# Kernel optimization log

Hardware: AMD Instinct MI355X
Metric: run time of the kernel (lower is better)

## Reference

```python
import jax, jax.numpy as jnp
import numpy as np

DIM = 64  # QK head dim, matches init kwarg 'dim'

def setup_inputs() -> dict:
    key = jax.random.key(0)
    kq, kk, kv = jax.random.split(key, 3)
    B, L, C, D, H = 2, 2048, 16, DIM, 64
    query = jax.random.normal(kq, (B, L, C, D), dtype=jnp.float32)
    k_ = jax.random.normal(kk, (B, L, C, D), dtype=jnp.float32)
    value = jax.random.normal(kv, (B, L, C, H), dtype=jnp.float32)
    return {"query": query, "key": k_, "value": value}

def reference(query, key, value):
    scaler = 1.0 / jnp.sqrt(jnp.float32(DIM))
    # score: [b, c, l, m]
    score = jnp.einsum('blcd,bmcd->bclm', query, key) * scaler
    # mask=False, dropout=0 -> identity
    attn = jax.nn.softmax(score, axis=3)
    # out: [b, l, c, h]
    out = jnp.einsum('bmch,bclm->blch', value, attn)
    return out
```

## Files before the change

kernel.cpp:

```cpp
#include <hip/hip_runtime.h>
#include <hip/hip_bf16.h>
#include <stdint.h>

#define B_ 2
#define L_ 2048
#define C_ 16
#define D_ 64
#define H_ 64
#define QBLK 128
#define KVBLK 64
#define NTILES 32
#define NTHREADS 256
#define NHEADS 32
#define TILE_ELEMS 4096
#define TENSOR_ELEMS (NHEADS * NTILES * TILE_ELEMS)

typedef __attribute__((ext_vector_type(8))) short bf16x8;
typedef __attribute__((ext_vector_type(16))) float f32x16;
typedef __attribute__((ext_vector_type(8))) unsigned short u16x8;

__device__ inline unsigned short f2bf(float f) {
  union { float f; unsigned int u; } v; v.f = f;
  unsigned int u = v.u;
  unsigned int r = (u + 0x7FFFu + ((u >> 16) & 1u)) >> 16;
  return (unsigned short)r;
}

__device__ inline float fast_exp2(float x) {
#if __has_builtin(__builtin_amdgcn_exp2f)
  return __builtin_amdgcn_exp2f(x);
#else
  return exp2f(x);
#endif
}

__device__ inline unsigned cvt_pk_bf16(float lo, float hi) {
  unsigned r;
  asm("v_cvt_pk_bf16_f32 %0, %1, %2" : "=v"(r) : "v"(lo), "v"(hi));
  return r;
}

__device__ inline void pl32swap(unsigned &x, unsigned &y) {
#if __has_builtin(__builtin_amdgcn_permlane32_swap)
  auto r = __builtin_amdgcn_permlane32_swap(x, y, false, false);
  x = r[0]; y = r[1];
#else
  asm("v_permlane32_swap_b32 %0, %1" : "+v"(x), "+&v"(y));
#endif
}

__device__ inline float xsum32(float v) {
  unsigned x = __float_as_uint(v), y = x;
  pl32swap(x, y);
  return __uint_as_float(x) + __uint_as_float(y);
}

__global__ __launch_bounds__(256) void prepack_kernel(
    const float* __restrict__ Kg, const float* __restrict__ Vg,
    unsigned short* __restrict__ Kb, unsigned short* __restrict__ Vb) {
  int idx = blockIdx.x * 256 + threadIdx.x;
  if (idx < 524288) {
    int i = idx;
    int lane = i & 63, frag = (i >> 6) & 7, t = (i >> 9) & 31, head = i >> 14;
    int b = head >> 4, c = head & 15;
    int ks = frag >> 1, half = frag & 1;
    int row = half * 32 + (lane & 31);
    int kb = ks * 16 + (lane >> 5) * 8;
    const float* src = Kg + ((size_t)(b * L_ + t * 64 + row) * C_ + c) * D_ + kb;
    float4 a0 = ((const float4*)src)[0];
    float4 a1 = ((const float4*)src)[1];
    u16x8 pk;
    pk[0] = f2bf(a0.x); pk[1] = f2bf(a0.y); pk[2] = f2bf(a0.z); pk[3] = f2bf(a0.w);
    pk[4] = f2bf(a1.x); pk[5] = f2bf(a1.y); pk[6] = f2bf(a1.z); pk[7] = f2bf(a1.w);
    size_t dst = ((((size_t)(head * 32 + t)) * 8 + frag) * 64 + lane) * 8;
    *(u16x8*)&Kb[dst] = pk;
  } else {
    int i = idx - 524288;
    int lane = i & 63, frag = (i >> 6) & 7, t = (i >> 9) & 31, head = i >> 14;
    int b = head >> 4, c = head & 15;
    int m = frag >> 1, half = frag & 1;
    int h = half * 32 + (lane & 31);
    int kv0 = m * 16 + (lane >> 5) * 8;
    const float* src = Vg + ((size_t)(b * L_ + t * 64 + kv0) * C_ + c) * H_ + h;
    u16x8 pv;
#pragma unroll
    for (int j = 0; j < 8; ++j) pv[j] = f2bf(src[(size_t)j * C_ * H_]);
    size_t dst = ((((size_t)(head * 32 + t)) * 8 + frag) * 64 + lane) * 8;
    *(u16x8*)&Vb[dst] = pv;
  }
}

__global__ __launch_bounds__(NTHREADS, 2) void attn_fwd_kernel(
    const float* __restrict__ Qg,
    const unsigned short* __restrict__ Kb,
    const unsigned short* __restrict__ Vb,
    float* __restrict__ Og) {
  const int tid  = threadIdx.x;
  const int lane = tid & 63;
  const int w    = tid >> 6;
  const int ql   = lane & 31;
  const int u    = lane >> 5;

  const int bid   = blockIdx.x;
  const int swz   = (bid & 7) * 64 + (bid >> 3);
  const int head  = swz >> 4;
  const int qtile = swz & 15;
  const int b     = head >> 4;
  const int c     = head & 15;
  const int q0    = qtile * QBLK;

  const unsigned short* KbL = Kb + (size_t)head * NTILES * TILE_ELEMS + lane * 8;
  const unsigned short* VbL = Vb + (size_t)head * NTILES * TILE_ELEMS + lane * 8;

  const float sc2 = 0.125f * 1.44269504088896340736f;
  const int qr = q0 + w * 32 + ql;
  const float* qrow = Qg + ((size_t)(b * L_ + qr) * C_ + c) * D_;
  bf16x8 qf[4];
#pragma unroll
  for (int ks = 0; ks < 4; ++ks) {
    float4 a0 = *(const float4*)(qrow + ks * 16 + u * 8);
    float4 a1 = *(const float4*)(qrow + ks * 16 + u * 8 + 4);
    bf16x8 q8;
    q8[0] = (short)f2bf(a0.x * sc2); q8[1] = (short)f2bf(a0.y * sc2);
    q8[2] = (short)f2bf(a0.z * sc2); q8[3] = (short)f2bf(a0.w * sc2);
    q8[4] = (short)f2bf(a1.x * sc2); q8[5] = (short)f2bf(a1.y * sc2);
    q8[6] = (short)f2bf(a1.z * sc2); q8[7] = (short)f2bf(a1.w * sc2);
    qf[ks] = q8;
  }

  f32x16 o0, o1;
#pragma unroll
  for (int i = 0; i < 16; ++i) { o0[i] = 0.f; o1[i] = 0.f; }
  float l_own = 0.f;

  bf16x8 kfr[8], vfr[8];
#pragma unroll
  for (int f = 0; f < 8; ++f) kfr[f] = *(const bf16x8*)(KbL + (size_t)f * 512);
#pragma unroll
  for (int f = 0; f < 8; ++f) vfr[f] = *(const bf16x8*)(VbL + (size_t)f * 512);

  for (int t = 0; t < NTILES; ++t) {
    const int tl = (t + 1 < NTILES) ? (t + 1) : t;

    f32x16 s0, s1;
#pragma unroll
    for (int i = 0; i < 16; ++i) { s0[i] = 0.f; s1[i] = 0.f; }
    __builtin_amdgcn_s_setprio(1);
#pragma unroll
    for (int ks = 0; ks < 4; ++ks) {
      s0 = __builtin_amdgcn_mfma_f32_32x32x16_bf16(kfr[2 * ks], qf[ks], s0, 0, 0, 0);
      s1 = __builtin_amdgcn_mfma_f32_32x32x16_bf16(kfr[2 * ks + 1], qf[ks], s1, 0, 0, 0);
    }
    __builtin_amdgcn_s_setprio(0);

#pragma unroll
    for (int f = 0; f < 8; ++f)
      kfr[f] = *(const bf16x8*)(KbL + (size_t)(tl * 8 + f) * 512);

    float rst[4];
    bf16x8 pf[4];
#pragma unroll
    for (int tq = 0; tq < 4; ++tq) {
      const int be = ((2 * tq) & 3) * 4;
      const int bo = ((2 * tq + 1) & 3) * 4;
      float p0[4], p1[4];
#pragma unroll
      for (int r = 0; r < 4; ++r) {
        float se = (tq < 2) ? s0[be + r] : s1[be + r];
        float so_ = (tq < 2) ? s0[bo + r] : s1[bo + r];
        p0[r] = fast_exp2(se);
        p1[r] = fast_exp2(so_);
      }
      rst[tq] = ((p0[0] + p0[1]) + (p0[2] + p0[3])) +
                ((p1[0] + p1[1]) + (p1[2] + p1[3]));
      unsigned x0 = cvt_pk_bf16(p0[0], p0[1]);
      unsigned x1 = cvt_pk_bf16(p0[2], p0[3]);
      unsigned y0 = cvt_pk_bf16(p1[0], p1[1]);
      unsigned y1 = cvt_pk_bf16(p1[2], p1[3]);
      pl32swap(x0, y0);
      pl32swap(x1, y1);
      union { unsigned wd[4]; bf16x8 v; } pk;
      pk.wd[0] = x0; pk.wd[1] = x1; pk.wd[2] = y0; pk.wd[3] = y1;
      pf[tq] = pk.v;
    }
    l_own += (rst[0] + rst[1]) + (rst[2] + rst[3]);

    __builtin_amdgcn_s_setprio(1);
#pragma unroll
    for (int m = 0; m < 4; ++m) {
      o0 = __builtin_amdgcn_mfma_f32_32x32x16_bf16(vfr[2 * m], pf[m], o0, 0, 0, 0);
      o1 = __builtin_amdgcn_mfma_f32_32x32x16_bf16(vfr[2 * m + 1], pf[m], o1, 0, 0, 0);
    }
    __builtin_amdgcn_s_setprio(0);

#pragma unroll
    for (int f = 0; f < 8; ++f)
      vfr[f] = *(const bf16x8*)(VbL + (size_t)(tl * 8 + f) * 512);
  }

  const float inv = 1.0f / xsum32(l_own);
  float* orow = Og + ((size_t)(b * L_ + qr) * C_ + c) * H_;
#pragma unroll
  for (int rg = 0; rg < 4; ++rg) {
    float4 v0, v1;
    v0.x = o0[rg * 4 + 0] * inv; v0.y = o0[rg * 4 + 1] * inv;
    v0.z = o0[rg * 4 + 2] * inv; v0.w = o0[rg * 4 + 3] * inv;
    v1.x = o1[rg * 4 + 0] * inv; v1.y = o1[rg * 4 + 1] * inv;
    v1.z = o1[rg * 4 + 2] * inv; v1.w = o1[rg * 4 + 3] * inv;
    *(float4*)(orow + 8 * rg + 4 * u) = v0;
    *(float4*)(orow + 32 + 8 * rg + 4 * u) = v1;
  }
}

extern "C" void kernel_launch(void* const* d_in, const int* in_sizes, int n_in,
                              void* d_out, int out_size, void* d_ws, size_t ws_size,
                              hipStream_t stream) {
  const float* Qg = (const float*)d_in[0];
  const float* Kg = (const float*)d_in[1];
  const float* Vg = (const float*)d_in[2];
  float* Og = (float*)d_out;

  unsigned short* Kb = (unsigned short*)d_ws;
  unsigned short* Vb = Kb + (size_t)TENSOR_ELEMS;

  prepack_kernel<<<4096, 256, 0, stream>>>(Kg, Vg, Kb, Vb);

  dim3 grid(NHEADS * (L_ / QBLK));
  dim3 block(NTHREADS);
  attn_fwd_kernel<<<grid, block, 0, stream>>>(Qg, Kb, Vb, Og);
}
```

Before: 59.74 us.

## Halve block size and drop register prefetch of K/V fragments for higher occupancy

Blocks shrink from 4 to 2 waves, covering 64 query rows each, and the grid doubles to keep the same total work. The 16-fragment double-buffered register prefetch of K and V for the next tile is replaced by on-demand loads of four fragments at a time just before each MFMA group. Launch bounds now ask for 4 blocks per CU, so register pressure drops and more waves can hide load latency. In exchange, each load's latency is no longer overlapped within a wave and is exposed right before its MFMAs, so the code relies on other waves to cover it.

```diff
diff --git a/kernel.cpp b/kernel.cpp
--- a/kernel.cpp
+++ b/kernel.cpp
@@ -7,10 +7,9 @@
 #define C_ 16
 #define D_ 64
 #define H_ 64
-#define QBLK 128
 #define KVBLK 64
 #define NTILES 32
-#define NTHREADS 256
+#define NTHREADS 128
 #define NHEADS 32
 #define TILE_ELEMS 4096
 #define TENSOR_ELEMS (NHEADS * NTILES * TILE_ELEMS)
@@ -90,7 +89,7 @@
   }
 }
 
-__global__ __launch_bounds__(NTHREADS, 2) void attn_fwd_kernel(
+__global__ __launch_bounds__(NTHREADS, 4) void attn_fwd_kernel(
     const float* __restrict__ Qg,
     const unsigned short* __restrict__ Kb,
     const unsigned short* __restrict__ Vb,
@@ -102,12 +101,12 @@
   const int u    = lane >> 5;
 
   const int bid   = blockIdx.x;
-  const int swz   = (bid & 7) * 64 + (bid >> 3);
-  const int head  = swz >> 4;
-  const int qtile = swz & 15;
+  const int swz   = (bid & 7) * 128 + (bid >> 3);
+  const int head  = swz >> 5;
+  const int qpair = swz & 31;
   const int b     = head >> 4;
   const int c     = head & 15;
-  const int q0    = qtile * QBLK;
+  const int q0    = qpair * 64;
 
   const unsigned short* KbL = Kb + (size_t)head * NTILES * TILE_ELEMS + lane * 8;
   const unsigned short* VbL = Vb + (size_t)head * NTILES * TILE_ELEMS + lane * 8;
@@ -133,29 +132,35 @@
   for (int i = 0; i < 16; ++i) { o0[i] = 0.f; o1[i] = 0.f; }
   float l_own = 0.f;
 
-  bf16x8 kfr[8], vfr[8];
-#pragma unroll
-  for (int f = 0; f < 8; ++f) kfr[f] = *(const bf16x8*)(KbL + (size_t)f * 512);
-#pragma unroll
-  for (int f = 0; f < 8; ++f) vfr[f] = *(const bf16x8*)(VbL + (size_t)f * 512);
-
   for (int t = 0; t < NTILES; ++t) {
-    const int tl = (t + 1 < NTILES) ? (t + 1) : t;
+    const unsigned short* Kt = KbL + (size_t)t * TILE_ELEMS;
+    const unsigned short* Vt = VbL + (size_t)t * TILE_ELEMS;
 
     f32x16 s0, s1;
 #pragma unroll
     for (int i = 0; i < 16; ++i) { s0[i] = 0.f; s1[i] = 0.f; }
-    __builtin_amdgcn_s_setprio(1);
-#pragma unroll
-    for (int ks = 0; ks < 4; ++ks) {
-      s0 = __builtin_amdgcn_mfma_f32_32x32x16_bf16(kfr[2 * ks], qf[ks], s0, 0, 0, 0);
-      s1 = __builtin_amdgcn_mfma_f32_32x32x16_bf16(kfr[2 * ks + 1], qf[ks], s1, 0, 0, 0);
+    {
+      bf16x8 k0_ = *(const bf16x8*)(Kt);
+      bf16x8 k1_ = *(const bf16x8*)(Kt + 512);
+      bf16x8 k2_ = *(const bf16x8*)(Kt + 1024);
+      bf16x8 k3_ = *(const bf16x8*)(Kt + 1536);
+      __builtin_amdgcn_s_setprio(1);
+      s0 = __builtin_amdgcn_mfma_f32_32x32x16_bf16(k0_, qf[0], s0, 0, 0, 0);
+      s1 = __builtin_amdgcn_mfma_f32_32x32x16_bf16(k1_, qf[0], s1, 0, 0, 0);
+      s0 = __builtin_amdgcn_mfma_f32_32x32x16_bf16(k2_, qf[1], s0, 0, 0, 0);
+      s1 = __builtin_amdgcn_mfma_f32_32x32x16_bf16(k3_, qf[1], s1, 0, 0, 0);
+      __builtin_amdgcn_s_setprio(0);
+      k0_ = *(const bf16x8*)(Kt + 2048);
+      k1_ = *(const bf16x8*)(Kt + 2560);
+      k2_ = *(const bf16x8*)(Kt + 3072);
+      k3_ = *(const bf16x8*)(Kt + 3584);
+      __builtin_amdgcn_s_setprio(1);
+      s0 = __builtin_amdgcn_mfma_f32_32x32x16_bf16(k0_, qf[2], s0, 0, 0, 0);
+      s1 = __builtin_amdgcn_mfma_f32_32x32x16_bf16(k1_, qf[2], s1, 0, 0, 0);
+      s0 = __builtin_amdgcn_mfma_f32_32x32x16_bf16(k2_, qf[3], s0, 0, 0, 0);
+      s1 = __builtin_amdgcn_mfma_f32_32x32x16_bf16(k3_, qf[3], s1, 0, 0, 0);
+      __builtin_amdgcn_s_setprio(0);
     }
-    __builtin_amdgcn_s_setprio(0);
-
-#pragma unroll
-    for (int f = 0; f < 8; ++f)
-      kfr[f] = *(const bf16x8*)(KbL + (size_t)(tl * 8 + f) * 512);
 
     float rst[4];
     bf16x8 pf[4];
@@ -185,17 +190,28 @@
     }
     l_own += (rst[0] + rst[1]) + (rst[2] + rst[3]);
 
-    __builtin_amdgcn_s_setprio(1);
-#pragma unroll
-    for (int m = 0; m < 4; ++m) {
-      o0 = __builtin_amdgcn_mfma_f32_32x32x16_bf16(vfr[2 * m], pf[m], o0, 0, 0, 0);
-      o1 = __builtin_amdgcn_mfma_f32_32x32x16_bf16(vfr[2 * m + 1], pf[m], o1, 0, 0, 0);
+    {
+      bf16x8 v0_ = *(const bf16x8*)(Vt);
+      bf16x8 v1_ = *(const bf16x8*)(Vt + 512);
+      bf16x8 v2_ = *(const bf16x8*)(Vt + 1024);
+      bf16x8 v3_ = *(const bf16x8*)(Vt + 1536);
+      __builtin_amdgcn_s_setprio(1);
+      o0 = __builtin_amdgcn_mfma_f32_32x32x16_bf16(v0_, pf[0], o0, 0, 0, 0);
+      o1 = __builtin_amdgcn_mfma_f32_32x32x16_bf16(v1_, pf[0], o1, 0, 0, 0);
+      o0 = __builtin_amdgcn_mfma_f32_32x32x16_bf16(v2_, pf[1], o0, 0, 0, 0);
+      o1 = __builtin_amdgcn_mfma_f32_32x32x16_bf16(v3_, pf[1], o1, 0, 0, 0);
+      __builtin_amdgcn_s_setprio(0);
+      v0_ = *(const bf16x8*)(Vt + 2048);
+      v1_ = *(const bf16x8*)(Vt + 2560);
+      v2_ = *(const bf16x8*)(Vt + 3072);
+      v3_ = *(const bf16x8*)(Vt + 3584);
+      __builtin_amdgcn_s_setprio(1);
+      o0 = __builtin_amdgcn_mfma_f32_32x32x16_bf16(v0_, pf[2], o0, 0, 0, 0);
+      o1 = __builtin_amdgcn_mfma_f32_32x32x16_bf16(v1_, pf[2], o1, 0, 0, 0);
+      o0 = __builtin_amdgcn_mfma_f32_32x32x16_bf16(v2_, pf[3], o0, 0, 0, 0);
+      o1 = __builtin_amdgcn_mfma_f32_32x32x16_bf16(v3_, pf[3], o1, 0, 0, 0);
+      __builtin_amdgcn_s_setprio(0);
     }
-    __builtin_amdgcn_s_setprio(0);
-
-#pragma unroll
-    for (int f = 0; f < 8; ++f)
-      vfr[f] = *(const bf16x8*)(VbL + (size_t)(tl * 8 + f) * 512);
   }
 
   const float inv = 1.0f / xsum32(l_own);
@@ -225,7 +241,7 @@
 
   prepack_kernel<<<4096, 256, 0, stream>>>(Kg, Vg, Kb, Vb);
 
-  dim3 grid(NHEADS * (L_ / QBLK));
+  dim3 grid(NHEADS * (L_ / 64));
   dim3 block(NTHREADS);
   attn_fwd_kernel<<<grid, block, 0, stream>>>(Qg, Kb, Vb, Og);
 }
```

Result: slower. 69.29 us (+16.0%).

## Software-pipeline QK^T MFMA of next tile with softmax of current tile

Applied to the files above, without the earlier changes.

Restructures the main loop so the QK^T MFMAs for tile t+1 are issued interleaved with the exp2/pack work for tile t, using double-buffered score accumulators (sA/sB) and a loop unrolled by two via a macro. K fragments are prefetched two tiles ahead and V one tile ahead. The aim is to hide the exp/convert VALU latency behind matrix-core work. In exchange it needs extra accumulator registers (32 more VGPRs), which could cause spills or lower occupancy at 2 waves per SIMD.

```diff
diff --git a/kernel.cpp b/kernel.cpp
--- a/kernel.cpp
+++ b/kernel.cpp
@@ -90,6 +90,60 @@
   }
 }
 
+#define TILE_BODY(SC0, SC1, SN0, SN1, T)                                          \
+  {                                                                               \
+    _Pragma("unroll")                                                             \
+    for (int z = 0; z < 16; ++z) { SN0[z] = 0.f; SN1[z] = 0.f; }                  \
+    float rst[4];                                                                 \
+    bf16x8 pf[4];                                                                 \
+    _Pragma("unroll")                                                             \
+    for (int i = 0; i < 4; ++i) {                                                 \
+      const int be = ((2 * i) & 3) * 4;                                           \
+      const int bo = ((2 * i + 1) & 3) * 4;                                       \
+      float p0[4], p1[4];                                                         \
+      _Pragma("unroll")                                                           \
+      for (int r = 0; r < 4; ++r) {                                               \
+        float se = (i < 2) ? SC0[be + r] : SC1[be + r];                           \
+        float so_ = (i < 2) ? SC0[bo + r] : SC1[bo + r];                          \
+        p0[r] = fast_exp2(se);                                                    \
+        p1[r] = fast_exp2(so_);                                                   \
+      }                                                                           \
+      rst[i] = ((p0[0] + p0[1]) + (p0[2] + p0[3])) +                              \
+               ((p1[0] + p1[1]) + (p1[2] + p1[3]));                               \
+      unsigned x0 = cvt_pk_bf16(p0[0], p0[1]);                                    \
+      unsigned x1 = cvt_pk_bf16(p0[2], p0[3]);                                    \
+      unsigned y0 = cvt_pk_bf16(p1[0], p1[1]);                                    \
+      unsigned y1 = cvt_pk_bf16(p1[2], p1[3]);                                    \
+      pl32swap(x0, y0);                                                           \
+      pl32swap(x1, y1);                                                           \
+      union { unsigned wd[4]; bf16x8 v; } pk_;                                    \
+      pk_.wd[0] = x0; pk_.wd[1] = x1; pk_.wd[2] = y0; pk_.wd[3] = y1;             \
+      pf[i] = pk_.v;                                                              \
+      SN0 = __builtin_amdgcn_mfma_f32_32x32x16_bf16(kf[2 * i], qf[i], SN0, 0, 0, 0);     \
+      SN1 = __builtin_amdgcn_mfma_f32_32x32x16_bf16(kf[2 * i + 1], qf[i], SN1, 0, 0, 0); \
+    }                                                                             \
+    l_own += (rst[0] + rst[1]) + (rst[2] + rst[3]);                               \
+    {                                                                             \
+      const int tk = ((T) + 2 < NTILES) ? (T) + 2 : NTILES - 1;                   \
+      _Pragma("unroll")                                                           \
+      for (int f = 0; f < 8; ++f)                                                 \
+        kf[f] = *(const bf16x8*)(KbL + (size_t)(tk * 8 + f) * 512);               \
+    }                                                                             \
+    __builtin_amdgcn_s_setprio(1);                                                \
+    _Pragma("unroll")                                                             \
+    for (int m = 0; m < 4; ++m) {                                                 \
+      o0 = __builtin_amdgcn_mfma_f32_32x32x16_bf16(vf[2 * m], pf[m], o0, 0, 0, 0);       \
+      o1 = __builtin_amdgcn_mfma_f32_32x32x16_bf16(vf[2 * m + 1], pf[m], o1, 0, 0, 0);   \
+    }                                                                             \
+    __builtin_amdgcn_s_setprio(0);                                                \
+    {                                                                             \
+      const int tv = ((T) + 1 < NTILES) ? (T) + 1 : NTILES - 1;                   \
+      _Pragma("unroll")                                                           \
+      for (int f = 0; f < 8; ++f)                                                 \
+        vf[f] = *(const bf16x8*)(VbL + (size_t)(tv * 8 + f) * 512);               \
+    }                                                                             \
+  }
+
 __global__ __launch_bounds__(NTHREADS, 2) void attn_fwd_kernel(
     const float* __restrict__ Qg,
     const unsigned short* __restrict__ Kb,
@@ -133,69 +187,29 @@
   for (int i = 0; i < 16; ++i) { o0[i] = 0.f; o1[i] = 0.f; }
   float l_own = 0.f;
 
-  bf16x8 kfr[8], vfr[8];
-#pragma unroll
-  for (int f = 0; f < 8; ++f) kfr[f] = *(const bf16x8*)(KbL + (size_t)f * 512);
-#pragma unroll
-  for (int f = 0; f < 8; ++f) vfr[f] = *(const bf16x8*)(VbL + (size_t)f * 512);
-
-  for (int t = 0; t < NTILES; ++t) {
-    const int tl = (t + 1 < NTILES) ? (t + 1) : t;
-
-    f32x16 s0, s1;
-#pragma unroll
-    for (int i = 0; i < 16; ++i) { s0[i] = 0.f; s1[i] = 0.f; }
-    __builtin_amdgcn_s_setprio(1);
-#pragma unroll
-    for (int ks = 0; ks < 4; ++ks) {
-      s0 = __builtin_amdgcn_mfma_f32_32x32x16_bf16(kfr[2 * ks], qf[ks], s0, 0, 0, 0);
-      s1 = __builtin_amdgcn_mfma_f32_32x32x16_bf16(kfr[2 * ks + 1], qf[ks], s1, 0, 0, 0);
-    }
-    __builtin_amdgcn_s_setprio(0);
-
-#pragma unroll
-    for (int f = 0; f < 8; ++f)
-      kfr[f] = *(const bf16x8*)(KbL + (size_t)(tl * 8 + f) * 512);
-
-    float rst[4];
-    bf16x8 pf[4];
-#pragma unroll
-    for (int tq = 0; tq < 4; ++tq) {
-      const int be = ((2 * tq) & 3) * 4;
-      const int bo = ((2 * tq + 1) & 3) * 4;
-      float p0[4], p1[4];
-#pragma unroll
-      for (int r = 0; r < 4; ++r) {
-        float se = (tq < 2) ? s0[be + r] : s1[be + r];
-        float so_ = (tq < 2) ? s0[bo + r] : s1[bo + r];
-        p0[r] = fast_exp2(se);
-        p1[r] = fast_exp2(so_);
-      }
-      rst[tq] = ((p0[0] + p0[1]) + (p0[2] + p0[3])) +
-                ((p1[0] + p1[1]) + (p1[2] + p1[3]));
-      unsigned x0 = cvt_pk_bf16(p0[0], p0[1]);
-      unsigned x1 = cvt_pk_bf16(p0[2], p0[3]);
-      unsigned y0 = cvt_pk_bf16(p1[0], p1[1]);
-      unsigned y1 = cvt_pk_bf16(p1[2], p1[3]);
-      pl32swap(x0, y0);
-      pl32swap(x1, y1);
-      union { unsigned wd[4]; bf16x8 v; } pk;
-      pk.wd[0] = x0; pk.wd[1] = x1; pk.wd[2] = y0; pk.wd[3] = y1;
-      pf[tq] = pk.v;
-    }
-    l_own += (rst[0] + rst[1]) + (rst[2] + rst[3]);
-
-    __builtin_amdgcn_s_setprio(1);
-#pragma unroll
-    for (int m = 0; m < 4; ++m) {
-      o0 = __builtin_amdgcn_mfma_f32_32x32x16_bf16(vfr[2 * m], pf[m], o0, 0, 0, 0);
-      o1 = __builtin_amdgcn_mfma_f32_32x32x16_bf16(vfr[2 * m + 1], pf[m], o1, 0, 0, 0);
-    }
-    __builtin_amdgcn_s_setprio(0);
-
-#pragma unroll
-    for (int f = 0; f < 8; ++f)
-      vfr[f] = *(const bf16x8*)(VbL + (size_t)(tl * 8 + f) * 512);
+  bf16x8 kf[8], vf[8];
+#pragma unroll
+  for (int f = 0; f < 8; ++f) kf[f] = *(const bf16x8*)(KbL + (size_t)f * 512);
+#pragma unroll
+  for (int f = 0; f < 8; ++f) vf[f] = *(const bf16x8*)(VbL + (size_t)f * 512);
+
+  f32x16 sA0, sA1, sB0, sB1;
+#pragma unroll
+  for (int i = 0; i < 16; ++i) { sA0[i] = 0.f; sA1[i] = 0.f; }
+  __builtin_amdgcn_s_setprio(1);
+#pragma unroll
+  for (int ks = 0; ks < 4; ++ks) {
+    sA0 = __builtin_amdgcn_mfma_f32_32x32x16_bf16(kf[2 * ks], qf[ks], sA0, 0, 0, 0);
+    sA1 = __builtin_amdgcn_mfma_f32_32x32x16_bf16(kf[2 * ks + 1], qf[ks], sA1, 0, 0, 0);
+  }
+  __builtin_amdgcn_s_setprio(0);
+#pragma unroll
+  for (int f = 0; f < 8; ++f)
+    kf[f] = *(const bf16x8*)(KbL + (size_t)(8 + f) * 512);
+
+  for (int t = 0; t < NTILES; t += 2) {
+    TILE_BODY(sA0, sA1, sB0, sB1, t);
+    TILE_BODY(sB0, sB1, sA0, sA1, t + 1);
   }
 
   const float inv = 1.0f / xsum32(l_own);
```

Result: faster. 57.32 us (-4.1%).

## Software-pipeline QK^T, softmax exp and PV MFMAs across KV tiles

Applied to the files above, without the earlier changes.

Restructures the attention main loop so that each step computes the score MFMAs for the next KV tile, runs the exp/pack for the current tile, and does the PV MFMAs for the previous tile, all interleaved. Two sets of score accumulators and P-fragment buffers ping-pong across a manually unrolled pair of iterations. K is prefetched two tiles ahead. The aim is to hide the exp and transcendental work behind MFMA latency. In exchange it costs more VGPRs, one wasted zero-P MFMA pass at the start and redundant score MFMAs on the clamped tail tiles, and it drops the s_setprio hints.

```diff
diff --git a/kernel.cpp b/kernel.cpp
--- a/kernel.cpp
+++ b/kernel.cpp
@@ -90,6 +90,51 @@
   }
 }
 
+#define QTR(TQ, SC0, SC1, SN0, SN1, PFI, PFO, KN_, VN_)                        \
+  {                                                                            \
+    SN0 = __builtin_amdgcn_mfma_f32_32x32x16_bf16(kf[2*TQ],   qf[TQ], SN0, 0, 0, 0); \
+    SN1 = __builtin_amdgcn_mfma_f32_32x32x16_bf16(kf[2*TQ+1], qf[TQ], SN1, 0, 0, 0); \
+    o0  = __builtin_amdgcn_mfma_f32_32x32x16_bf16(vf[2*TQ],   PFI[TQ], o0, 0, 0, 0); \
+    o1  = __builtin_amdgcn_mfma_f32_32x32x16_bf16(vf[2*TQ+1], PFI[TQ], o1, 0, 0, 0); \
+    kf[2*TQ]   = *(const bf16x8*)((KN_) + (2*TQ) * 512);                       \
+    kf[2*TQ+1] = *(const bf16x8*)((KN_) + (2*TQ+1) * 512);                     \
+    vf[2*TQ]   = *(const bf16x8*)((VN_) + (2*TQ) * 512);                       \
+    vf[2*TQ+1] = *(const bf16x8*)((VN_) + (2*TQ+1) * 512);                     \
+    const int be = ((2*TQ) & 3) * 4, bo = ((2*TQ+1) & 3) * 4;                  \
+    float p0[4], p1[4];                                                        \
+    _Pragma("unroll")                                                          \
+    for (int r = 0; r < 4; ++r) {                                              \
+      float se  = (TQ < 2) ? SC0[be + r] : SC1[be + r];                        \
+      float so_ = (TQ < 2) ? SC0[bo + r] : SC1[bo + r];                        \
+      p0[r] = fast_exp2(se);                                                   \
+      p1[r] = fast_exp2(so_);                                                  \
+    }                                                                          \
+    l_own += ((p0[0]+p0[1]) + (p0[2]+p0[3])) + ((p1[0]+p1[1]) + (p1[2]+p1[3]));\
+    unsigned x0 = cvt_pk_bf16(p0[0], p0[1]);                                   \
+    unsigned x1 = cvt_pk_bf16(p0[2], p0[3]);                                   \
+    unsigned y0 = cvt_pk_bf16(p1[0], p1[1]);                                   \
+    unsigned y1 = cvt_pk_bf16(p1[2], p1[3]);                                   \
+    pl32swap(x0, y0);                                                          \
+    pl32swap(x1, y1);                                                          \
+    union { unsigned wd[4]; bf16x8 v; } pk_;                                   \
+    pk_.wd[0] = x0; pk_.wd[1] = x1; pk_.wd[2] = y0; pk_.wd[3] = y1;            \
+    PFO[TQ] = pk_.v;                                                           \
+  }
+
+#define BODY(SC0, SC1, SN0, SN1, PFI, PFO, T)                                  \
+  {                                                                            \
+    const int t_ = (T);                                                        \
+    const int tk_ = (t_ + 2 < NTILES) ? t_ + 2 : NTILES - 1;                   \
+    const unsigned short* KN_ = KbL + (size_t)tk_ * TILE_ELEMS;                \
+    const unsigned short* VN_ = VbL + (size_t)t_ * TILE_ELEMS;                 \
+    _Pragma("unroll")                                                          \
+    for (int z = 0; z < 16; ++z) { SN0[z] = 0.f; SN1[z] = 0.f; }               \
+    QTR(0, SC0, SC1, SN0, SN1, PFI, PFO, KN_, VN_)                             \
+    QTR(1, SC0, SC1, SN0, SN1, PFI, PFO, KN_, VN_)                             \
+    QTR(2, SC0, SC1, SN0, SN1, PFI, PFO, KN_, VN_)                             \
+    QTR(3, SC0, SC1, SN0, SN1, PFI, PFO, KN_, VN_)                             \
+  }
+
 __global__ __launch_bounds__(NTHREADS, 2) void attn_fwd_kernel(
     const float* __restrict__ Qg,
     const unsigned short* __restrict__ Kb,
@@ -133,69 +178,36 @@
   for (int i = 0; i < 16; ++i) { o0[i] = 0.f; o1[i] = 0.f; }
   float l_own = 0.f;
 
-  bf16x8 kfr[8], vfr[8];
-#pragma unroll
-  for (int f = 0; f < 8; ++f) kfr[f] = *(const bf16x8*)(KbL + (size_t)f * 512);
-#pragma unroll
-  for (int f = 0; f < 8; ++f) vfr[f] = *(const bf16x8*)(VbL + (size_t)f * 512);
-
-  for (int t = 0; t < NTILES; ++t) {
-    const int tl = (t + 1 < NTILES) ? (t + 1) : t;
-
-    f32x16 s0, s1;
-#pragma unroll
-    for (int i = 0; i < 16; ++i) { s0[i] = 0.f; s1[i] = 0.f; }
-    __builtin_amdgcn_s_setprio(1);
-#pragma unroll
-    for (int ks = 0; ks < 4; ++ks) {
-      s0 = __builtin_amdgcn_mfma_f32_32x32x16_bf16(kfr[2 * ks], qf[ks], s0, 0, 0, 0);
-      s1 = __builtin_amdgcn_mfma_f32_32x32x16_bf16(kfr[2 * ks + 1], qf[ks], s1, 0, 0, 0);
-    }
-    __builtin_amdgcn_s_setprio(0);
-
-#pragma unroll
-    for (int f = 0; f < 8; ++f)
-      kfr[f] = *(const bf16x8*)(KbL + (size_t)(tl * 8 + f) * 512);
-
-    float rst[4];
-    bf16x8 pf[4];
-#pragma unroll
-    for (int tq = 0; tq < 4; ++tq) {
-      const int be = ((2 * tq) & 3) * 4;
-      const int bo = ((2 * tq + 1) & 3) * 4;
-      float p0[4], p1[4];
-#pragma unroll
-      for (int r = 0; r < 4; ++r) {
-        float se = (tq < 2) ? s0[be + r] : s1[be + r];
-        float so_ = (tq < 2) ? s0[bo + r] : s1[bo + r];
-        p0[r] = fast_exp2(se);
-        p1[r] = fast_exp2(so_);
-      }
-      rst[tq] = ((p0[0] + p0[1]) + (p0[2] + p0[3])) +
-                ((p1[0] + p1[1]) + (p1[2] + p1[3]));
-      unsigned x0 = cvt_pk_bf16(p0[0], p0[1]);
-      unsigned x1 = cvt_pk_bf16(p0[2], p0[3]);
-      unsigned y0 = cvt_pk_bf16(p1[0], p1[1]);
-      unsigned y1 = cvt_pk_bf16(p1[2], p1[3]);
-      pl32swap(x0, y0);
-      pl32swap(x1, y1);
-      union { unsigned wd[4]; bf16x8 v; } pk;
-      pk.wd[0] = x0; pk.wd[1] = x1; pk.wd[2] = y0; pk.wd[3] = y1;
-      pf[tq] = pk.v;
-    }
-    l_own += (rst[0] + rst[1]) + (rst[2] + rst[3]);
-
-    __builtin_amdgcn_s_setprio(1);
-#pragma unroll
-    for (int m = 0; m < 4; ++m) {
-      o0 = __builtin_amdgcn_mfma_f32_32x32x16_bf16(vfr[2 * m], pf[m], o0, 0, 0, 0);
-      o1 = __builtin_amdgcn_mfma_f32_32x32x16_bf16(vfr[2 * m + 1], pf[m], o1, 0, 0, 0);
-    }
-    __builtin_amdgcn_s_setprio(0);
-
-#pragma unroll
-    for (int f = 0; f < 8; ++f)
-      vfr[f] = *(const bf16x8*)(VbL + (size_t)(tl * 8 + f) * 512);
+  f32x16 sX0, sX1, sY0, sY1;
+  bf16x8 kf[8], vf[8], pfA[4], pfB[4];
+
+#pragma unroll
+  for (int f = 0; f < 8; ++f) kf[f] = *(const bf16x8*)(KbL + (size_t)f * 512);
+#pragma unroll
+  for (int i = 0; i < 16; ++i) { sX0[i] = 0.f; sX1[i] = 0.f; }
+#pragma unroll
+  for (int ks = 0; ks < 4; ++ks) {
+    sX0 = __builtin_amdgcn_mfma_f32_32x32x16_bf16(kf[2*ks],   qf[ks], sX0, 0, 0, 0);
+    sX1 = __builtin_amdgcn_mfma_f32_32x32x16_bf16(kf[2*ks+1], qf[ks], sX1, 0, 0, 0);
+  }
+#pragma unroll
+  for (int f = 0; f < 8; ++f)
+    kf[f] = *(const bf16x8*)(KbL + (size_t)(8 + f) * 512);
+#pragma unroll
+  for (int f = 0; f < 8; ++f)
+    vf[f] = *(const bf16x8*)(VbL + (size_t)f * 512);
+#pragma unroll
+  for (int m = 0; m < 4; ++m) pfA[m] = (bf16x8)(short)0;
+
+  for (int p = 0; p < 16; ++p) {
+    BODY(sX0, sX1, sY0, sY1, pfA, pfB, 2 * p);
+    BODY(sY0, sY1, sX0, sX1, pfB, pfA, 2 * p + 1);
+  }
+
+#pragma unroll
+  for (int m = 0; m < 4; ++m) {
+    o0 = __builtin_amdgcn_mfma_f32_32x32x16_bf16(vf[2*m],   pfA[m], o0, 0, 0, 0);
+    o1 = __builtin_amdgcn_mfma_f32_32x32x16_bf16(vf[2*m+1], pfA[m], o1, 0, 0, 0);
   }
 
   const float inv = 1.0f / xsum32(l_own);
```

Result: no change. 59.59 us (-0.3%).
